# Performance work log

Hardware: AMD Instinct MI355X
Metric: run time of the kernel (lower is better)

## Reference

```python
import jax, jax.numpy as jnp
import numpy as np

HEADS = 16

def setup_inputs() -> dict:
    key = jax.random.key(0)
    k1, k2, k3 = jax.random.split(key, 3)
    B, S, D = 2, 2048, 1024
    return {
        "query": jax.random.normal(k1, (B, S, D), dtype=jnp.float32),
        "key": jax.random.normal(k2, (B, S, D), dtype=jnp.float32),
        "value": jax.random.normal(k3, (B, S, D), dtype=jnp.float32),
    }

def reference(query, key, value):
    B, S, D = query.shape
    H = HEADS
    dh = D // H
    # split(-1) into H equal chunks == reshape to (B, S, H, dh)
    q = query.reshape(B, S, H, dh)
    k = key.reshape(B, S, H, dh)
    v = value.reshape(B, S, H, dh)
    scale = 1.0 / jnp.sqrt(jnp.asarray(dh, dtype=query.dtype))
    scores = jnp.einsum('bqhd,bkhd->bhqk', q, k) * scale  # [B,H,S,S]
    probs = jax.nn.softmax(scores, axis=-1)
    out = jnp.einsum('bhqk,bkhd->bqhd', probs, v)  # [B,S,H,dh]
    return out.reshape(B, S, D)
```

## Files before the change

kernel.cpp:

```cpp
#include <hip/hip_runtime.h>
#include <stdint.h>


#define B_ 2
#define S_ 2048
#define D_ 1024
#define H_ 16
#define DH 64
#define M_TILE 128
#define N_TILE 128
#define NITER (S_ / N_TILE)

typedef __bf16 bf16;
typedef __bf16 bf16x2 __attribute__((ext_vector_type(2)));
typedef __bf16 bf16x4 __attribute__((ext_vector_type(4)));
typedef __bf16 bf16x8 __attribute__((ext_vector_type(8)));
typedef float floatx4 __attribute__((ext_vector_type(4)));

#define KB_HEAD (S_ * DH * 2)
#define KB_TOTAL (B_ * H_ * KB_HEAD)
#define VT_ROW (S_ * 2)
#define WS_NEEDED (2u * KB_TOTAL)

#define KTILE_B 16384
#define BUF_B 32768
#define LSH_OFF 65536
#define SMEM_MAIN (LSH_OFF + 512)
#define O_STRIDE 36

__device__ __forceinline__ float fast_exp2(float x) {
#if __has_builtin(__builtin_amdgcn_exp2f)
  return __builtin_amdgcn_exp2f(x);
#else
  return exp2f(x);
#endif
}

__device__ __forceinline__ void gl_lds16(const void* g, void* l) {
  __builtin_amdgcn_global_load_lds(
      (const __attribute__((address_space(1))) unsigned int*)g,
      (__attribute__((address_space(3))) unsigned int*)l, 16, 0, 0);
}

__global__ __launch_bounds__(256)
void prep(const float* __restrict__ Kg, const float* __restrict__ Vg,
          unsigned char* __restrict__ ws) {
  const int bid = blockIdx.x;
  const int tid = threadIdx.x;
  if (bid < 512) {
    __shared__ __align__(16) bf16 VTsh[64][136];
    const int head_lin = bid & 31, ktile = bid >> 5;
    const int b = head_lin >> 4, h = head_lin & 15;
    const int kb = ktile * 128;
    const int vr0 = (tid >> 3) << 2;
    const int vf0 = (tid & 7) << 3;
    const float* Vbase = Vg + (size_t)(b * S_) * D_ + h * DH;
    float vals[4][8];
#pragma unroll
    for (int rr = 0; rr < 4; ++rr) {
      const float* vp = Vbase + (size_t)(kb + vr0 + rr) * D_ + vf0;
      float4 a = *(const float4*)vp;
      float4 c = *(const float4*)(vp + 4);
      vals[rr][0] = a.x; vals[rr][1] = a.y; vals[rr][2] = a.z; vals[rr][3] = a.w;
      vals[rr][4] = c.x; vals[rr][5] = c.y; vals[rr][6] = c.z; vals[rr][7] = c.w;
    }
    const int pbase = (vr0 & 96) + ((vr0 >> 2) & 3) * 8 + ((vr0 >> 4) & 1) * 4;
    const int psw = (((pbase >> 3) ^ (tid & 7)) << 3) | (pbase & 7);
#pragma unroll
    for (int j = 0; j < 8; ++j) {
      bf16x4 y = {(bf16)vals[0][j], (bf16)vals[1][j], (bf16)vals[2][j], (bf16)vals[3][j]};
      *(bf16x4*)(&VTsh[vf0 + j][psw]) = y;
    }
    __syncthreads();
    unsigned char* Vout = ws + KB_TOTAL + (size_t)head_lin * KB_HEAD;
#pragma unroll
    for (int j = 0; j < 4; ++j) {
      const int id  = j * 256 + tid;
      const int c   = id & 63;
      const int sub = id >> 6;
      const int fg  = sub & 3;
      const int ckl = sub >> 2;
      const int col = c & 15, quad = c >> 4;
      const int f = fg * 16 + col;
      const int g = ckl * 4 + quad;
      const int gs = g ^ ((f >> 3) & 7);
      bf16x8 v = *(const bf16x8*)(&VTsh[f][gs << 3]);
      *(bf16x8*)(Vout + (size_t)f * VT_ROW + kb * 2 + (ckl * 64 + quad * 16)) = v;
    }
  } else {
    const int idx = (bid - 512) * 256 + tid;
    const int f8 = idx & 7;
    const int s  = (idx >> 3) & 2047;
    const int hh = (idx >> 14) & 15;
    const int bb = idx >> 18;
    const float* src = Kg + (size_t)(bb * 2048 + s) * 1024 + hh * 64 + f8 * 8;
    float4 x0 = ((const float4*)src)[0];
    float4 x1 = ((const float4*)src)[1];
    bf16x8 y = {(bf16)x0.x, (bf16)x0.y, (bf16)x0.z, (bf16)x0.w,
                (bf16)x1.x, (bf16)x1.y, (bf16)x1.z, (bf16)x1.w};
    *(bf16x8*)(ws + (size_t)idx * 16) = y;
  }
}

__global__ __launch_bounds__(512, 4)
void attn_fwd(const float* __restrict__ Qg, const unsigned char* __restrict__ Kb,
              const unsigned char* __restrict__ VT, float* __restrict__ Og) {
  __shared__ __align__(16) unsigned char smem[SMEM_MAIN];
  float* Osh = (float*)smem;
  float* Lsh = (float*)(smem + LSH_OFF);

  const int tid  = threadIdx.x;
  const int lane = tid & 63;
  const int wave = tid >> 6;
  const int kw   = wave & 1;
  const int qw   = wave >> 1;
  const int col  = lane & 15;
  const int quad = lane >> 4;

  const int bid      = blockIdx.x;
  const int head_lin = bid & 31;
  const int qtile    = bid >> 5;
  const int b        = head_lin >> 4;
  const int h        = head_lin & 15;

  const unsigned char* Khead = Kb + (size_t)head_lin * KB_HEAD;
  const unsigned char* Vhead = VT + (size_t)head_lin * (DH * VT_ROW);

  const float QSCALE = 0.125f * 1.44269504088896340736f;

  bf16x8 Qf[2][2];
#pragma unroll
  for (int qt = 0; qt < 2; ++qt) {
    const float* base = Qg + (size_t)(b * S_ + qtile * M_TILE + qw * 32 + qt * 16 + col) * D_
                        + h * DH + quad * 8;
#pragma unroll
    for (int ks = 0; ks < 2; ++ks) {
      float4 x0 = *(const float4*)(base + ks * 32);
      float4 x1 = *(const float4*)(base + ks * 32 + 4);
      bf16x8 f;
      f[0] = (bf16)(x0.x * QSCALE); f[1] = (bf16)(x0.y * QSCALE);
      f[2] = (bf16)(x0.z * QSCALE); f[3] = (bf16)(x0.w * QSCALE);
      f[4] = (bf16)(x1.x * QSCALE); f[5] = (bf16)(x1.y * QSCALE);
      f[6] = (bf16)(x1.z * QSCALE); f[7] = (bf16)(x1.w * QSCALE);
      Qf[qt][ks] = f;
    }
  }

  floatx4 accO[4][2];
  float l_lane[2] = {0.f, 0.f};
#pragma unroll
  for (int ft = 0; ft < 4; ++ft)
#pragma unroll
    for (int qt = 0; qt < 2; ++qt) accO[ft][qt] = (floatx4)0.f;

  const int krow_b = wave * 16 + (lane >> 3);
  const int kcg    = lane & 7;
  const int vf_b   = wave * 8 + (lane >> 4);
  const int vcg    = lane & 15;

  const int krow0   = kw * 64 + col;
  const int ka0_off = krow0 * 128 + ((quad ^ (col & 7)) << 4);
  const int ka1_off = krow0 * 128 + (((quad | 4) ^ (col & 7)) << 4);
  const int va_c0   = KTILE_B + col * 256 + ((((kw << 3) | quad) ^ col) << 4);
  const int va_c1   = KTILE_B + col * 256 + ((((kw << 3) | 4 | quad) ^ col) << 4);

  auto dma_tile = [&](int kbk, int bufoff) {
#pragma unroll
    for (int t = 0; t < 2; ++t) {
      const int r = krow_b + t * 8;
      gl_lds16(Khead + (size_t)(kbk + r) * 128 + ((kcg ^ (r & 7)) << 4),
               smem + bufoff + (wave * 16 + t * 8) * 128);
    }
#pragma unroll
    for (int t = 0; t < 2; ++t) {
      const int f = vf_b + t * 4;
      gl_lds16(Vhead + (size_t)f * VT_ROW + kbk * 2 + ((vcg ^ (f & 15)) << 4),
               smem + bufoff + KTILE_B + (wave * 8 + t * 4) * 256);
    }
  };

  dma_tile(0, 0);
  __syncthreads();

  for (int it = 0; it < NITER; ++it) {
    const int bc = (it & 1) << 15;
    if (it + 1 < NITER) dma_tile((it + 1) * N_TILE, bc ^ BUF_B);

    floatx4 accS[4][2];
#pragma unroll
    for (int kt = 0; kt < 4; ++kt) {
      bf16x8 Ka0 = *(const bf16x8*)(smem + bc + ka0_off + kt * 2048);
      bf16x8 Ka1 = *(const bf16x8*)(smem + bc + ka1_off + kt * 2048);
#pragma unroll
      for (int qt = 0; qt < 2; ++qt) {
        floatx4 a = (floatx4)0.f;
        a = __builtin_amdgcn_mfma_f32_16x16x32_bf16(Ka0, Qf[qt][0], a, 0, 0, 0);
        a = __builtin_amdgcn_mfma_f32_16x16x32_bf16(Ka1, Qf[qt][1], a, 0, 0, 0);
        accS[kt][qt] = a;
      }
    }

#pragma unroll
    for (int qt = 0; qt < 2; ++qt) {
      float rs = 0.f;
#pragma unroll
      for (int kt = 0; kt < 4; ++kt)
#pragma unroll
        for (int r = 0; r < 4; ++r) {
          float p = fast_exp2(accS[kt][qt][r]);
          accS[kt][qt][r] = p;
          rs += p;
        }
      l_lane[qt] += rs;
    }

#pragma unroll
    for (int c = 0; c < 2; ++c) {
      bf16x8 Pf[2];
#pragma unroll
      for (int qt = 0; qt < 2; ++qt) {
        floatx4 p0 = accS[2 * c][qt], p1 = accS[2 * c + 1][qt];
        bf16x8 f = {(bf16)p0[0], (bf16)p0[1], (bf16)p0[2], (bf16)p0[3],
                    (bf16)p1[0], (bf16)p1[1], (bf16)p1[2], (bf16)p1[3]};
        Pf[qt] = f;
      }
      const int vo = c ? va_c1 : va_c0;
#pragma unroll
      for (int ft = 0; ft < 4; ++ft) {
        bf16x8 Va = *(const bf16x8*)(smem + bc + vo + ft * 4096);
#pragma unroll
        for (int qt = 0; qt < 2; ++qt)
          accO[ft][qt] = __builtin_amdgcn_mfma_f32_16x16x32_bf16(Va, Pf[qt], accO[ft][qt], 0, 0, 0);
      }
    }
    __syncthreads();
  }

  float l_red[2];
#pragma unroll
  for (int qt = 0; qt < 2; ++qt) {
    float s = l_lane[qt];
    s += __shfl_xor(s, 16);
    s += __shfl_xor(s, 32);
    l_red[qt] = s;
  }

  if (kw == 1) {
    float* r = Osh + (qw * 64 + lane) * O_STRIDE;
#pragma unroll
    for (int qt = 0; qt < 2; ++qt)
#pragma unroll
      for (int ft = 0; ft < 4; ++ft)
        *(floatx4*)(r + (qt * 4 + ft) * 4) = accO[ft][qt];
    if (quad == 0) {
#pragma unroll
      for (int qt = 0; qt < 2; ++qt)
        Lsh[qw * 32 + qt * 16 + col] = l_red[qt];
    }
  }
  __syncthreads();

  if (kw == 0) {
    const float* r = Osh + (qw * 64 + lane) * O_STRIDE;
    float rl[2];
#pragma unroll
    for (int qt = 0; qt < 2; ++qt)
      rl[qt] = 1.0f / (l_red[qt] + Lsh[qw * 32 + qt * 16 + col]);
#pragma unroll
    for (int qt = 0; qt < 2; ++qt) {
      const int q = qtile * M_TILE + qw * 32 + qt * 16 + col;
      float* dst = Og + (size_t)(b * S_ + q) * D_ + h * DH + quad * 4;
#pragma unroll
      for (int ft = 0; ft < 4; ++ft) {
        floatx4 o = (accO[ft][qt] + *(const floatx4*)(r + (qt * 4 + ft) * 4)) * rl[qt];
        *(floatx4*)(dst + ft * 16) = o;
      }
    }
  }
}

#define FB_K_STRIDE 68
#define FB_V_STRIDE 132
#define FB_K_BYTES (128 * FB_K_STRIDE * 2)
#define FB_V_BYTES (64 * FB_V_STRIDE * 2)
#define FB_SMEM ((256 * O_STRIDE * 4 + 2048) > (FB_K_BYTES + FB_V_BYTES) ? (256 * O_STRIDE * 4 + 2048) : (FB_K_BYTES + FB_V_BYTES))

__device__ __forceinline__ bf16x8 cat8(bf16x4 a, bf16x4 b) {
  return __builtin_shufflevector(a, b, 0, 1, 2, 3, 4, 5, 6, 7);
}

__global__ __launch_bounds__(512, 4)
void attn_fwd_fb(const float* __restrict__ Qg, const float* __restrict__ Kg,
                 const float* __restrict__ Vg, float* __restrict__ Og) {
  __shared__ __align__(16) unsigned char smem[FB_SMEM];
  bf16*  Ksh = (bf16*)smem;
  bf16*  Vsh = (bf16*)(smem + FB_K_BYTES);
  float* Osh = (float*)smem;
  float* Lsh = (float*)(smem + 256 * O_STRIDE * 4);

  const int tid  = threadIdx.x;
  const int lane = tid & 63;
  const int wave = tid >> 6;
  const int kw   = wave & 1;
  const int qw   = wave >> 1;
  const int col  = lane & 15;
  const int quad = lane >> 4;
  const int bid      = blockIdx.x;
  const int head_lin = bid & 31;
  const int qtile    = bid >> 5;
  const int b        = head_lin >> 4;
  const int h        = head_lin & 15;
  const float QSCALE = 0.125f * 1.44269504088896340736f;

  bf16x8 Qf[2][2];
#pragma unroll
  for (int qt = 0; qt < 2; ++qt) {
    const float* base = Qg + (size_t)(b * S_ + qtile * 128 + qw * 32 + qt * 16 + col) * D_
                        + h * DH + quad * 8;
#pragma unroll
    for (int ks = 0; ks < 2; ++ks) {
      float4 x0 = *(const float4*)(base + ks * 32);
      float4 x1 = *(const float4*)(base + ks * 32 + 4);
      bf16x8 f;
      f[0] = (bf16)(x0.x * QSCALE); f[1] = (bf16)(x0.y * QSCALE);
      f[2] = (bf16)(x0.z * QSCALE); f[3] = (bf16)(x0.w * QSCALE);
      f[4] = (bf16)(x1.x * QSCALE); f[5] = (bf16)(x1.y * QSCALE);
      f[6] = (bf16)(x1.z * QSCALE); f[7] = (bf16)(x1.w * QSCALE);
      Qf[qt][ks] = f;
    }
  }

  floatx4 accO[4][2];
  float l_lane[2] = {0.f, 0.f};
#pragma unroll
  for (int ft = 0; ft < 4; ++ft)
#pragma unroll
    for (int qt = 0; qt < 2; ++qt) accO[ft][qt] = (floatx4)0.f;

  const float* Kbase = Kg + (size_t)(b * S_) * D_ + h * DH;
  const float* Vbase = Vg + (size_t)(b * S_) * D_ + h * DH;
  const int krow0 = tid >> 4;
  const int kf4   = tid & 15;
  const int vk0   = (tid >> 3) * 2;
  const int vf0   = (tid & 7) * 8;

  for (int it = 0; it < NITER; ++it) {
    const int kb = it * 128;
    float4 kx[4];
#pragma unroll
    for (int i = 0; i < 4; ++i)
      kx[i] = *(const float4*)(Kbase + (size_t)(kb + krow0 + 32 * i) * D_ + kf4 * 4);
    float4 va0 = *(const float4*)(Vbase + (size_t)(kb + vk0) * D_ + vf0);
    float4 va1 = *(const float4*)(Vbase + (size_t)(kb + vk0) * D_ + vf0 + 4);
    float4 vb0 = *(const float4*)(Vbase + (size_t)(kb + vk0 + 1) * D_ + vf0);
    float4 vb1 = *(const float4*)(Vbase + (size_t)(kb + vk0 + 1) * D_ + vf0 + 4);
#pragma unroll
    for (int i = 0; i < 4; ++i) {
      bf16x4 y = {(bf16)kx[i].x, (bf16)kx[i].y, (bf16)kx[i].z, (bf16)kx[i].w};
      *(bf16x4*)(Ksh + (krow0 + 32 * i) * FB_K_STRIDE + kf4 * 4) = y;
    }
    {
      float a[8] = {va0.x, va0.y, va0.z, va0.w, va1.x, va1.y, va1.z, va1.w};
      float c[8] = {vb0.x, vb0.y, vb0.z, vb0.w, vb1.x, vb1.y, vb1.z, vb1.w};
#pragma unroll
      for (int j = 0; j < 8; ++j) {
        bf16x2 y = {(bf16)a[j], (bf16)c[j]};
        *(bf16x2*)(Vsh + (vf0 + j) * FB_V_STRIDE + vk0) = y;
      }
    }
    __syncthreads();

    floatx4 accS[4][2];
#pragma unroll
    for (int kt = 0; kt < 4; ++kt) {
      const bf16* kp = Ksh + (kw * 64 + kt * 16 + col) * FB_K_STRIDE + quad * 8;
      bf16x8 Ka0 = cat8(*(const bf16x4*)kp, *(const bf16x4*)(kp + 4));
      bf16x8 Ka1 = cat8(*(const bf16x4*)(kp + 32), *(const bf16x4*)(kp + 36));
#pragma unroll
      for (int qt = 0; qt < 2; ++qt) {
        floatx4 a = (floatx4)0.f;
        a = __builtin_amdgcn_mfma_f32_16x16x32_bf16(Ka0, Qf[qt][0], a, 0, 0, 0);
        a = __builtin_amdgcn_mfma_f32_16x16x32_bf16(Ka1, Qf[qt][1], a, 0, 0, 0);
        accS[kt][qt] = a;
      }
    }
#pragma unroll
    for (int qt = 0; qt < 2; ++qt) {
      float rs = 0.f;
#pragma unroll
      for (int kt = 0; kt < 4; ++kt)
#pragma unroll
        for (int r = 0; r < 4; ++r) {
          float p = fast_exp2(accS[kt][qt][r]);
          accS[kt][qt][r] = p;
          rs += p;
        }
      l_lane[qt] += rs;
    }
#pragma unroll
    for (int c = 0; c < 2; ++c) {
      bf16x8 Pf[2];
#pragma unroll
      for (int qt = 0; qt < 2; ++qt) {
        floatx4 p0 = accS[2 * c][qt], p1 = accS[2 * c + 1][qt];
        bf16x8 f = {(bf16)p0[0], (bf16)p0[1], (bf16)p0[2], (bf16)p0[3],
                    (bf16)p1[0], (bf16)p1[1], (bf16)p1[2], (bf16)p1[3]};
        Pf[qt] = f;
      }
#pragma unroll
      for (int ft = 0; ft < 4; ++ft) {
        const bf16* vp = Vsh + (ft * 16 + col) * FB_V_STRIDE + kw * 64 + 32 * c + quad * 4;
        bf16x8 Va = cat8(*(const bf16x4*)vp, *(const bf16x4*)(vp + 16));
#pragma unroll
        for (int qt = 0; qt < 2; ++qt)
          accO[ft][qt] = __builtin_amdgcn_mfma_f32_16x16x32_bf16(Va, Pf[qt], accO[ft][qt], 0, 0, 0);
      }
    }
    __syncthreads();
  }

  float l_red[2];
#pragma unroll
  for (int qt = 0; qt < 2; ++qt) {
    float s = l_lane[qt];
    s += __shfl_xor(s, 16);
    s += __shfl_xor(s, 32);
    l_red[qt] = s;
  }
  if (kw == 1) {
    float* r = Osh + (qw * 64 + lane) * O_STRIDE;
#pragma unroll
    for (int qt = 0; qt < 2; ++qt)
#pragma unroll
      for (int ft = 0; ft < 4; ++ft)
        *(floatx4*)(r + (qt * 4 + ft) * 4) = accO[ft][qt];
    if (quad == 0) {
#pragma unroll
      for (int qt = 0; qt < 2; ++qt)
        Lsh[qw * 32 + qt * 16 + col] = l_red[qt];
    }
  }
  __syncthreads();
  if (kw == 0) {
    const float* r = Osh + (qw * 64 + lane) * O_STRIDE;
    float rl[2];
#pragma unroll
    for (int qt = 0; qt < 2; ++qt)
      rl[qt] = 1.0f / (l_red[qt] + Lsh[qw * 32 + qt * 16 + col]);
#pragma unroll
    for (int qt = 0; qt < 2; ++qt) {
      const int q = qtile * 128 + qw * 32 + qt * 16 + col;
      float* dst = Og + (size_t)(b * S_ + q) * D_ + h * DH + quad * 4;
#pragma unroll
      for (int ft = 0; ft < 4; ++ft) {
        floatx4 o = (accO[ft][qt] + *(const floatx4*)(r + (qt * 4 + ft) * 4)) * rl[qt];
        *(floatx4*)(dst + ft * 16) = o;
      }
    }
  }
}

extern "C" void kernel_launch(void* const* d_in, const int* in_sizes, int n_in,
                              void* d_out, int out_size, void* d_ws, size_t ws_size,
                              hipStream_t stream) {
  const float* Q = (const float*)d_in[0];
  const float* K = (const float*)d_in[1];
  const float* V = (const float*)d_in[2];
  float* O = (float*)d_out;
  if (ws_size >= WS_NEEDED && d_ws != nullptr) {
    unsigned char* ws = (unsigned char*)d_ws;
    hipLaunchKernelGGL(prep, dim3(2560), dim3(256), 0, stream, K, V, ws);
    hipLaunchKernelGGL(attn_fwd, dim3(B_ * H_ * (S_ / M_TILE)), dim3(512), 0, stream,
                       Q, ws, ws + KB_TOTAL, O);
  } else {
    hipLaunchKernelGGL(attn_fwd_fb, dim3(512), dim3(512), 0, stream, Q, K, V, O);
  }
}
```

Before: 130.0 us.

## Switch to triple-buffered 64-key tiles with explicit vmcnt waits and setprio

New measurement: 130.1 us. No clear change (+0.1%).

```diff
diff --git a/kernel.cpp b/kernel.cpp
--- a/kernel.cpp
+++ b/kernel.cpp
@@ -22,10 +22,12 @@
 #define VT_ROW (S_ * 2)
 #define WS_NEEDED (2u * KB_TOTAL)
 
-#define KTILE_B 16384
-#define BUF_B 32768
-#define LSH_OFF 65536
-#define SMEM_MAIN (LSH_OFF + 512)
+#define N_TILE2 64
+#define NITER2 (S_ / N_TILE2)
+#define KT2 8192
+#define BUF2 16384
+#define LSH_OFF2 (3 * BUF2)
+#define SMEM_MAIN (LSH_OFF2 + 512)
 #define O_STRIDE 36
 
 __device__ __forceinline__ float fast_exp2(float x) {
@@ -107,7 +109,7 @@
               const unsigned char* __restrict__ VT, float* __restrict__ Og) {
   __shared__ __align__(16) unsigned char smem[SMEM_MAIN];
   float* Osh = (float*)smem;
-  float* Lsh = (float*)(smem + LSH_OFF);
+  float* Lsh = (float*)(smem + LSH_OFF2);
 
   const int tid  = threadIdx.x;
   const int lane = tid & 63;
@@ -153,42 +155,45 @@
 #pragma unroll
     for (int qt = 0; qt < 2; ++qt) accO[ft][qt] = (floatx4)0.f;
 
-  const int krow_b = wave * 16 + (lane >> 3);
-  const int kcg    = lane & 7;
-  const int vf_b   = wave * 8 + (lane >> 4);
-  const int vcg    = lane & 15;
-
-  const int krow0   = kw * 64 + col;
-  const int ka0_off = krow0 * 128 + ((quad ^ (col & 7)) << 4);
-  const int ka1_off = krow0 * 128 + (((quad | 4) ^ (col & 7)) << 4);
-  const int va_c0   = KTILE_B + col * 256 + ((((kw << 3) | quad) ^ col) << 4);
-  const int va_c1   = KTILE_B + col * 256 + ((((kw << 3) | 4 | quad) ^ col) << 4);
-
-  auto dma_tile = [&](int kbk, int bufoff) {
-#pragma unroll
-    for (int t = 0; t < 2; ++t) {
-      const int r = krow_b + t * 8;
-      gl_lds16(Khead + (size_t)(kbk + r) * 128 + ((kcg ^ (r & 7)) << 4),
-               smem + bufoff + (wave * 16 + t * 8) * 128);
-    }
-#pragma unroll
-    for (int t = 0; t < 2; ++t) {
-      const int f = vf_b + t * 4;
-      gl_lds16(Vhead + (size_t)f * VT_ROW + kbk * 2 + ((vcg ^ (f & 15)) << 4),
-               smem + bufoff + KTILE_B + (wave * 8 + t * 4) * 256);
-    }
+  const int sub = lane >> 3;
+  const int gx  = ((lane & 7) ^ sub) << 4;
+
+  auto dma_tile2 = [&](int kbk, int bufoff) {
+    const int r = (wave << 3) + sub;
+    gl_lds16(Khead + (size_t)(kbk + r) * 128 + gx,
+             smem + bufoff + (wave << 10));
+    gl_lds16(Vhead + (size_t)r * VT_ROW + kbk * 2 + gx,
+             smem + bufoff + KT2 + (wave << 10));
   };
 
-  dma_tile(0, 0);
-  __syncthreads();
-
-  for (int it = 0; it < NITER; ++it) {
-    const int bc = (it & 1) << 15;
-    if (it + 1 < NITER) dma_tile((it + 1) * N_TILE, bc ^ BUF_B);
-
-    floatx4 accS[4][2];
-#pragma unroll
-    for (int kt = 0; kt < 4; ++kt) {
+  const int cq = col & 7;
+  const int ka0_off = (kw * 32 + col) * 128 + ((quad ^ cq) << 4);
+  const int ka1_off = (kw * 32 + col) * 128 + (((quad | 4) ^ cq) << 4);
+  const int va0_off = KT2 + col * 128 + (((kw * 4 + quad) ^ cq) << 4);
+
+  dma_tile2(0, 0);
+  dma_tile2(N_TILE2, BUF2);
+
+  int bc = 0;
+  int bd = 2 * BUF2;
+
+  for (int it = 0; it < NITER2; ++it) {
+    if (it + 2 < NITER2) {
+      dma_tile2((it + 2) * N_TILE2, bd);
+      bd += BUF2; if (bd == 3 * BUF2) bd = 0;
+    }
+    __builtin_amdgcn_sched_barrier(0);
+    if (it + 2 < NITER2)       asm volatile("s_waitcnt vmcnt(4)" ::: "memory");
+    else if (it + 2 == NITER2) asm volatile("s_waitcnt vmcnt(2)" ::: "memory");
+    else                       asm volatile("s_waitcnt vmcnt(0)" ::: "memory");
+    __builtin_amdgcn_s_barrier();
+    asm volatile("" ::: "memory");
+    __builtin_amdgcn_sched_barrier(0);
+
+    floatx4 accS[2][2];
+    __builtin_amdgcn_s_setprio(1);
+#pragma unroll
+    for (int kt = 0; kt < 2; ++kt) {
       bf16x8 Ka0 = *(const bf16x8*)(smem + bc + ka0_off + kt * 2048);
       bf16x8 Ka1 = *(const bf16x8*)(smem + bc + ka1_off + kt * 2048);
 #pragma unroll
@@ -199,12 +204,13 @@
         accS[kt][qt] = a;
       }
     }
+    __builtin_amdgcn_s_setprio(0);
 
 #pragma unroll
     for (int qt = 0; qt < 2; ++qt) {
       float rs = 0.f;
 #pragma unroll
-      for (int kt = 0; kt < 4; ++kt)
+      for (int kt = 0; kt < 2; ++kt)
 #pragma unroll
         for (int r = 0; r < 4; ++r) {
           float p = fast_exp2(accS[kt][qt][r]);
@@ -214,27 +220,30 @@
       l_lane[qt] += rs;
     }
 
-#pragma unroll
-    for (int c = 0; c < 2; ++c) {
-      bf16x8 Pf[2];
-#pragma unroll
-      for (int qt = 0; qt < 2; ++qt) {
-        floatx4 p0 = accS[2 * c][qt], p1 = accS[2 * c + 1][qt];
-        bf16x8 f = {(bf16)p0[0], (bf16)p0[1], (bf16)p0[2], (bf16)p0[3],
-                    (bf16)p1[0], (bf16)p1[1], (bf16)p1[2], (bf16)p1[3]};
-        Pf[qt] = f;
-      }
-      const int vo = c ? va_c1 : va_c0;
-#pragma unroll
-      for (int ft = 0; ft < 4; ++ft) {
-        bf16x8 Va = *(const bf16x8*)(smem + bc + vo + ft * 4096);
-#pragma unroll
-        for (int qt = 0; qt < 2; ++qt)
-          accO[ft][qt] = __builtin_amdgcn_mfma_f32_16x16x32_bf16(Va, Pf[qt], accO[ft][qt], 0, 0, 0);
-      }
-    }
-    __syncthreads();
-  }
+    bf16x8 Pf[2];
+#pragma unroll
+    for (int qt = 0; qt < 2; ++qt) {
+      floatx4 p0 = accS[0][qt], p1 = accS[1][qt];
+      bf16x8 f = {(bf16)p0[0], (bf16)p0[1], (bf16)p0[2], (bf16)p0[3],
+                  (bf16)p1[0], (bf16)p1[1], (bf16)p1[2], (bf16)p1[3]};
+      Pf[qt] = f;
+    }
+    __builtin_amdgcn_s_setprio(1);
+#pragma unroll
+    for (int ft = 0; ft < 4; ++ft) {
+      bf16x8 Va = *(const bf16x8*)(smem + bc + va0_off + ft * 2048);
+#pragma unroll
+      for (int qt = 0; qt < 2; ++qt)
+        accO[ft][qt] = __builtin_amdgcn_mfma_f32_16x16x32_bf16(Va, Pf[qt], accO[ft][qt], 0, 0, 0);
+    }
+    __builtin_amdgcn_s_setprio(0);
+
+    __builtin_amdgcn_sched_barrier(0);
+    asm volatile("" ::: "memory");
+    __builtin_amdgcn_s_barrier();
+    bc += BUF2; if (bc == 3 * BUF2) bc = 0;
+  }
+  __syncthreads();
 
   float l_red[2];
 #pragma unroll
```

## Load K and V fragments directly from global memory instead of LDS staging

Applied to the files above, without the earlier changes.

Result: slower. 209.5 us (+61.2%).

```diff
diff --git a/kernel.cpp b/kernel.cpp
--- a/kernel.cpp
+++ b/kernel.cpp
@@ -22,11 +22,9 @@
 #define VT_ROW (S_ * 2)
 #define WS_NEEDED (2u * KB_TOTAL)
 
-#define KTILE_B 16384
-#define BUF_B 32768
-#define LSH_OFF 65536
-#define SMEM_MAIN (LSH_OFF + 512)
 #define O_STRIDE 36
+#define EPI_OSH (256 * O_STRIDE * 4)
+#define SMEM_MAIN (EPI_OSH + 512)
 
 __device__ __forceinline__ float fast_exp2(float x) {
 #if __has_builtin(__builtin_amdgcn_exp2f)
@@ -34,12 +32,6 @@
 #else
   return exp2f(x);
 #endif
-}
-
-__device__ __forceinline__ void gl_lds16(const void* g, void* l) {
-  __builtin_amdgcn_global_load_lds(
-      (const __attribute__((address_space(1))) unsigned int*)g,
-      (__attribute__((address_space(3))) unsigned int*)l, 16, 0, 0);
 }
 
 __global__ __launch_bounds__(256)
@@ -107,7 +99,7 @@
               const unsigned char* __restrict__ VT, float* __restrict__ Og) {
   __shared__ __align__(16) unsigned char smem[SMEM_MAIN];
   float* Osh = (float*)smem;
-  float* Lsh = (float*)(smem + LSH_OFF);
+  float* Lsh = (float*)(smem + EPI_OSH);
 
   const int tid  = threadIdx.x;
   const int lane = tid & 63;
@@ -153,44 +145,19 @@
 #pragma unroll
     for (int qt = 0; qt < 2; ++qt) accO[ft][qt] = (floatx4)0.f;
 
-  const int krow_b = wave * 16 + (lane >> 3);
-  const int kcg    = lane & 7;
-  const int vf_b   = wave * 8 + (lane >> 4);
-  const int vcg    = lane & 15;
-
-  const int krow0   = kw * 64 + col;
-  const int ka0_off = krow0 * 128 + ((quad ^ (col & 7)) << 4);
-  const int ka1_off = krow0 * 128 + (((quad | 4) ^ (col & 7)) << 4);
-  const int va_c0   = KTILE_B + col * 256 + ((((kw << 3) | quad) ^ col) << 4);
-  const int va_c1   = KTILE_B + col * 256 + ((((kw << 3) | 4 | quad) ^ col) << 4);
-
-  auto dma_tile = [&](int kbk, int bufoff) {
-#pragma unroll
-    for (int t = 0; t < 2; ++t) {
-      const int r = krow_b + t * 8;
-      gl_lds16(Khead + (size_t)(kbk + r) * 128 + ((kcg ^ (r & 7)) << 4),
-               smem + bufoff + (wave * 16 + t * 8) * 128);
-    }
-#pragma unroll
-    for (int t = 0; t < 2; ++t) {
-      const int f = vf_b + t * 4;
-      gl_lds16(Vhead + (size_t)f * VT_ROW + kbk * 2 + ((vcg ^ (f & 15)) << 4),
-               smem + bufoff + KTILE_B + (wave * 8 + t * 4) * 256);
-    }
-  };
-
-  dma_tile(0, 0);
-  __syncthreads();
+  const unsigned char* Kp = Khead + (size_t)((kw * 64 + col) * 128 + quad * 16);
+  const unsigned char* Vp = Vhead + (size_t)(col * 4096 + (((kw << 3) | quad) << 4));
 
   for (int it = 0; it < NITER; ++it) {
-    const int bc = (it & 1) << 15;
-    if (it + 1 < NITER) dma_tile((it + 1) * N_TILE, bc ^ BUF_B);
+    const unsigned char* kp = Kp + (size_t)it * (N_TILE * 128);
+    const unsigned char* vp = Vp + (size_t)it * (N_TILE * 2);
 
     floatx4 accS[4][2];
+    __builtin_amdgcn_s_setprio(1);
 #pragma unroll
     for (int kt = 0; kt < 4; ++kt) {
-      bf16x8 Ka0 = *(const bf16x8*)(smem + bc + ka0_off + kt * 2048);
-      bf16x8 Ka1 = *(const bf16x8*)(smem + bc + ka1_off + kt * 2048);
+      bf16x8 Ka0 = *(const bf16x8*)(kp + kt * 2048);
+      bf16x8 Ka1 = *(const bf16x8*)(kp + kt * 2048 + 64);
 #pragma unroll
       for (int qt = 0; qt < 2; ++qt) {
         floatx4 a = (floatx4)0.f;
@@ -199,6 +166,7 @@
         accS[kt][qt] = a;
       }
     }
+    __builtin_amdgcn_s_setprio(0);
 
 #pragma unroll
     for (int qt = 0; qt < 2; ++qt) {
@@ -224,16 +192,16 @@
                     (bf16)p1[0], (bf16)p1[1], (bf16)p1[2], (bf16)p1[3]};
         Pf[qt] = f;
       }
-      const int vo = c ? va_c1 : va_c0;
+      __builtin_amdgcn_s_setprio(1);
 #pragma unroll
       for (int ft = 0; ft < 4; ++ft) {
-        bf16x8 Va = *(const bf16x8*)(smem + bc + vo + ft * 4096);
+        bf16x8 Va = *(const bf16x8*)(vp + ft * 65536 + c * 64);
 #pragma unroll
         for (int qt = 0; qt < 2; ++qt)
           accO[ft][qt] = __builtin_amdgcn_mfma_f32_16x16x32_bf16(Va, Pf[qt], accO[ft][qt], 0, 0, 0);
       }
-    }
-    __syncthreads();
+      __builtin_amdgcn_s_setprio(0);
+    }
   }
 
   float l_red[2];
```
